# Performance work log

Measured on AMD Instinct MI355X. Metric: run time of the kernel, lower is better.

## Reference

```python
import jax, jax.numpy as jnp
import numpy as np

B, L, V, E, H, T = 64, 512, 30000, 256, 256, 9
H2 = H // 2


def setup_inputs() -> dict:
    key = jax.random.key(0)
    ks = jax.random.split(key, 16)
    s = 0.1
    sentence = jax.random.randint(ks[0], (B, L), 0, V)
    tags = jax.random.randint(ks[1], (B, L), 0, T)
    lengths = jax.random.randint(ks[2], (B,), L // 4, L + 1)
    padding_mask = (jnp.arange(L)[None, :] < lengths[:, None]).astype(jnp.int32)
    emb = jax.random.normal(ks[3], (V, E)) * s
    w_ih_f = jax.random.normal(ks[4], (4 * H2, E)) * s
    w_hh_f = jax.random.normal(ks[5], (4 * H2, H2)) * s
    b_f = jax.random.normal(ks[6], (4 * H2,)) * s
    w_ih_b = jax.random.normal(ks[7], (4 * H2, E)) * s
    w_hh_b = jax.random.normal(ks[8], (4 * H2, H2)) * s
    b_b = jax.random.normal(ks[9], (4 * H2,)) * s
    W_out = jax.random.normal(ks[10], (T, H)) * s
    b_out = jax.random.normal(ks[11], (T,)) * s
    start_trans = jax.random.normal(ks[12], (T,)) * s
    end_trans = jax.random.normal(ks[13], (T,)) * s
    trans = jax.random.normal(ks[14], (T, T)) * s
    return {"sentence": sentence, "tags": tags, "padding_mask": padding_mask,
            "batch_sequence_max_len": L, "emb": emb,
            "w_ih_f": w_ih_f, "w_hh_f": w_hh_f, "b_f": b_f,
            "w_ih_b": w_ih_b, "w_hh_b": w_hh_b, "b_b": b_b,
            "W_out": W_out, "b_out": b_out,
            "start_trans": start_trans, "end_trans": end_trans, "trans": trans}


def _lstm_dir(x, m, w_ih, w_hh, b):
    # x: [L,B,E] time-major, m: [L,B] bool. PyTorch gate order i,f,g,o.
    gx = jnp.einsum('lbe,ge->lbg', x, w_ih) + b  # precompute input contribution
    h2 = w_hh.shape[1]
    Bb = x.shape[1]

    def step(carry, inp):
        h, c = carry
        g, mt = inp
        g = g + h @ w_hh.T
        i, f, gg, o = jnp.split(g, 4, axis=-1)
        i = jax.nn.sigmoid(i); f = jax.nn.sigmoid(f)
        gg = jnp.tanh(gg); o = jax.nn.sigmoid(o)
        c_new = f * c + i * gg
        h_new = o * jnp.tanh(c_new)
        mt = mt[:, None]
        h_out = jnp.where(mt, h_new, h)
        c_out = jnp.where(mt, c_new, c)
        y = jnp.where(mt, h_new, 0.0)  # pad_packed pads outputs with 0
        return (h_out, c_out), y

    init = (jnp.zeros((Bb, h2), x.dtype), jnp.zeros((Bb, h2), x.dtype))
    _, outs = jax.lax.scan(step, init, (gx, m))
    return outs  # [L,B,H2]


def reference(sentence, tags, padding_mask, batch_sequence_max_len,
              emb, w_ih_f, w_hh_f, b_f, w_ih_b, w_hh_b, b_b,
              W_out, b_out, start_trans, end_trans, trans):
    Lm = batch_sequence_max_len
    sentence = sentence[:, :Lm]
    tags = tags[:, :Lm]
    pm = padding_mask[:, :Lm]
    Bsz = sentence.shape[0]
    bidx = jnp.arange(Bsz)

    x = jnp.swapaxes(emb[sentence], 0, 1)            # [L,B,E]
    m = jnp.swapaxes(pm, 0, 1).astype(bool)          # [L,B]
    fwd = _lstm_dir(x, m, w_ih_f, w_hh_f, b_f)
    bwd = _lstm_dir(x[::-1], m[::-1], w_ih_b, w_hh_b, b_b)[::-1]
    lstm_out = jnp.concatenate([fwd, bwd], axis=-1)  # [L,B,H]
    emissions = lstm_out @ W_out.T + b_out           # [L,B,T]

    tags_t = jnp.swapaxes(tags, 0, 1)                # [L,B]
    mf = m.astype(emissions.dtype)

    # ---- CRF numerator (gold path score) ----
    e_tag = jnp.take_along_axis(emissions, tags_t[:, :, None], axis=2)[:, :, 0]  # [L,B]
    num = start_trans[tags_t[0]] + e_tag[0]
    tr = trans[tags_t[:-1], tags_t[1:]]              # [L-1,B]
    num = num + jnp.sum((tr + e_tag[1:]) * mf[1:], axis=0)
    last_idx = jnp.sum(pm, axis=1).astype(jnp.int32) - 1
    num = num + end_trans[tags_t[last_idx, bidx]]

    # ---- CRF log-partition (forward algorithm) ----
    score0 = start_trans[None, :] + emissions[0]     # [B,T]

    def norm_step(score, inp):
        e_t, mt = inp
        nxt = jax.scipy.special.logsumexp(
            score[:, :, None] + trans[None, :, :] + e_t[:, None, :], axis=1)
        return jnp.where(mt[:, None], nxt, score), None

    score, _ = jax.lax.scan(norm_step, score0, (emissions[1:], m[1:]))
    logZ = jax.scipy.special.logsumexp(score + end_trans[None, :], axis=1)
    loss = -jnp.sum(num - logZ) / Bsz

    # ---- Viterbi decode (no mask, like module's self.crf.decode(lstm_feats)) ----
    def vit_step(score_v, e_t):
        cand = score_v[:, :, None] + trans[None, :, :] + e_t[:, None, :]  # [B,T,T]
        return jnp.max(cand, axis=1), jnp.argmax(cand, axis=1)

    vscore, hist = jax.lax.scan(vit_step, score0, emissions[1:])  # hist: [L-1,B,T]
    best_last = jnp.argmax(vscore + end_trans[None, :], axis=1)   # [B]

    def back_step(tag, h):
        return h[bidx, tag], tag

    first_tag, rest = jax.lax.scan(back_step, best_last, hist, reverse=True)
    path = jnp.concatenate([first_tag[None, :], rest], axis=0)    # [L,B]
    predict = jnp.swapaxes(path, 0, 1).astype(jnp.int32) * pm     # mask padded positions
    return loss, predict
```

## Files before the change

kernel.cpp:

```cpp
#include <hip/hip_runtime.h>
#include <math.h>

#define LSEQ 512
#define BATCH 64
#define EDIM 256
#define HD 128
#define G4 512
#define NTAG 9
#define MTOT (LSEQ*BATCH)

typedef _Float16 f16x8 __attribute__((ext_vector_type(8)));
typedef float    f32x4 __attribute__((ext_vector_type(4)));

__device__ __forceinline__ float fsig(float x){
    return __builtin_amdgcn_rcpf(1.0f + __expf(-x));
}
__device__ __forceinline__ float ftanh(float x){
    return 1.0f - 2.0f*__builtin_amdgcn_rcpf(1.0f + __expf(2.0f*x));
}
__device__ __forceinline__ void wg_barrier_lds(){
    asm volatile("s_waitcnt lgkmcnt(0)" ::: "memory");
    __builtin_amdgcn_s_barrier();
    asm volatile("" ::: "memory");
}

#define GBM 128
#define GBN 128
#define GBK 32
__global__ __launch_bounds__(256) void gx_gemm(
    const int* __restrict__ sent, const float* __restrict__ emb,
    const float* __restrict__ wf, const float* __restrict__ wb,
    const float* __restrict__ bf, const float* __restrict__ bb,
    float* __restrict__ gx)
{
    __shared__ f16x8 Ah[512], Am[512], Bh[512], Bm[512];
    __shared__ int sidx[GBM];
    const int tid = threadIdx.x;
    const int bm0 = blockIdx.x * GBM;
    const int bn0 = blockIdx.y * GBN;
    if (tid < GBM){
        int m = bm0 + tid;
        sidx[tid] = sent[(m & 63)*LSEQ + (m >> 6)];
    }
    __syncthreads();

    const float* srcA[2];
    const float* srcB[2];
    #pragma unroll
    for (int p=0;p<2;p++){
        const int d   = tid + 256*p;
        const int row = (d>>6)*16 + (d&15);
        const int kq  = (d>>4)&3;
        srcA[p] = emb + (size_t)sidx[row]*EDIM + kq*8;
        const int col = bn0 + row;
        srcB[p] = ((col < G4) ? (wf + (size_t)col*EDIM)
                              : (wb + (size_t)(col-G4)*EDIM)) + kq*8;
    }

    const int lane = tid & 63;
    const int wid  = tid >> 6;
    const int wm   = wid >> 1;
    const int wn   = wid & 1;

    f32x4 acc[4][4];
    #pragma unroll
    for (int i=0;i<4;i++)
        #pragma unroll
        for (int jj=0;jj<4;jj++)
            #pragma unroll
            for (int e=0;e<4;e++) acc[i][jj][e]=0.f;

    float4 ra[2][2], rb[2][2];
    #define LOADC(K0)  { _Pragma("unroll") for (int p=0;p<2;p++){ \
        ra[p][0] = *(const float4*)(srcA[p] + (K0));  ra[p][1] = *(const float4*)(srcA[p] + (K0) + 4); \
        rb[p][0] = *(const float4*)(srcB[p] + (K0));  rb[p][1] = *(const float4*)(srcB[p] + (K0) + 4); } }

    LOADC(0);
    for (int c=0;c<8;c++){
        wg_barrier_lds();
        #pragma unroll
        for (int p=0;p<2;p++){
            float va[8] = {ra[p][0].x, ra[p][0].y, ra[p][0].z, ra[p][0].w,
                           ra[p][1].x, ra[p][1].y, ra[p][1].z, ra[p][1].w};
            float vb[8] = {rb[p][0].x, rb[p][0].y, rb[p][0].z, rb[p][0].w,
                           rb[p][1].x, rb[p][1].y, rb[p][1].z, rb[p][1].w};
            f16x8 ahh, amm, bhh, bmm;
            #pragma unroll
            for (int i=0;i<8;i++){
                _Float16 hv = (_Float16)va[i];
                ahh[i] = hv; amm[i] = (_Float16)(va[i] - (float)hv);
                _Float16 hw = (_Float16)vb[i];
                bhh[i] = hw; bmm[i] = (_Float16)(vb[i] - (float)hw);
            }
            Ah[tid + 256*p] = ahh;  Am[tid + 256*p] = amm;
            Bh[tid + 256*p] = bhh;  Bm[tid + 256*p] = bmm;
        }
        if (c < 7) LOADC(32*(c+1));
        wg_barrier_lds();

        f16x8 ah[4], am[4];
        #pragma unroll
        for (int mt=0;mt<4;mt++){
            ah[mt] = Ah[(wm*4+mt)*64 + lane];
            am[mt] = Am[(wm*4+mt)*64 + lane];
        }
        #pragma unroll
        for (int nt=0;nt<4;nt++){
            f16x8 bh = Bh[(wn*4+nt)*64 + lane];
            f16x8 bm = Bm[(wn*4+nt)*64 + lane];
            #pragma unroll
            for (int mt=0;mt<4;mt++){
                acc[mt][nt] = __builtin_amdgcn_mfma_f32_16x16x32_f16(ah[mt], bh, acc[mt][nt], 0,0,0);
                acc[mt][nt] = __builtin_amdgcn_mfma_f32_16x16x32_f16(am[mt], bh, acc[mt][nt], 0,0,0);
                acc[mt][nt] = __builtin_amdgcn_mfma_f32_16x16x32_f16(ah[mt], bm, acc[mt][nt], 0,0,0);
            }
        }
    }
    #undef LOADC

    #pragma unroll
    for (int mt=0;mt<4;mt++){
        #pragma unroll
        for (int nt=0;nt<4;nt++){
            const int n   = bn0 + wn*64 + nt*16 + (lane & 15);
            const int dir = n >> 9;
            const int j   = n & 511;
            const float bias = (n < G4) ? bf[n] : bb[n - G4];
            const int mrow = bm0 + wm*64 + mt*16 + ((lane >> 4) << 2);
            float* o = gx + (size_t)dir*((size_t)MTOT*G4) + (size_t)mrow*G4 + j;
            o[0*G4] = acc[mt][nt][0] + bias;
            o[1*G4] = acc[mt][nt][1] + bias;
            o[2*G4] = acc[mt][nt][2] + bias;
            o[3*G4] = acc[mt][nt][3] + bias;
        }
    }
}

__global__ __launch_bounds__(512, 2) void lstm_rec(
    const float* __restrict__ gx,
    const float* __restrict__ whf, const float* __restrict__ whb,
    const int* __restrict__ pm,
    float* __restrict__ lout)
{
    const int wg  = blockIdx.x;
    const int dir = wg >> 6;
    const int b   = wg & 63;
    const int t   = threadIdx.x;
    const int kh  = t >> 8;
    const int gr  = t & 255;
    const int j   = t & 127;

    const float* wbase = dir ? whb : whf;
    float w0[64], w1[64];
    {
        const float* r0 = wbase + (size_t)gr*HD       + kh*64;
        const float* r1 = wbase + (size_t)(gr+256)*HD + kh*64;
        #pragma unroll
        for (int k=0;k<64;k+=4){
            float4 v = *(const float4*)(r0+k);
            w0[k]=v.x; w0[k+1]=v.y; w0[k+2]=v.z; w0[k+3]=v.w;
            float4 u = *(const float4*)(r1+k);
            w1[k]=u.x; w1[k+1]=u.y; w1[k+2]=u.z; w1[k+3]=u.w;
        }
    }
    __shared__ float hsh[HD];
    __shared__ float pact[2][512];
    __shared__ int   pms[LSEQ];
    for (int q=t; q<LSEQ; q+=512) pms[q] = pm[b*LSEQ + q];
    if (t < HD) hsh[t] = 0.f;
    float c = 0.f, h = 0.f;

    const size_t stepel = (size_t)BATCH*G4;
    const float* gxb = gx + (size_t)dir*((size_t)MTOT*G4) + (size_t)b*G4
                          + (dir ? (size_t)(LSEQ-1)*stepel : 0);
    const ptrdiff_t dstep = dir ? -(ptrdiff_t)stepel : (ptrdiff_t)stepel;
    float* op = lout + (size_t)b*256 + dir*HD + j;

    float4 gc = {0,0,0,0}, gn1 = {0,0,0,0};
    if (t < 128){
        gc.x  = gxb[j];          gc.y  = gxb[j+128];
        gc.z  = gxb[j+256];      gc.w  = gxb[j+384];
        const float* p1 = gxb + dstep;
        gn1.x = p1[j];           gn1.y = p1[j+128];
        gn1.z = p1[j+256];       gn1.w = p1[j+384];
    }
    wg_barrier_lds();

    for (int s=0; s<LSEQ; s++){
        float4 gn2 = {0,0,0,0};
        if (t < 128 && s+2 < LSEQ){
            const float* p = gxb + (ptrdiff_t)(s+2)*dstep;
            gn2.x = p[j]; gn2.y = p[j+128]; gn2.z = p[j+256]; gn2.w = p[j+384];
        }
        const int l = dir ? (LSEQ-1-s) : s;
        const int pmv = pms[l];

        float a0=0.f,a1=0.f,b0=0.f,b1=0.f;
        const float* hp = &hsh[kh*64];
        #pragma unroll
        for (int k=0;k<64;k+=8){
            float4 x0 = *(const float4*)(hp+k);
            float4 x1 = *(const float4*)(hp+k+4);
            a0 += x0.x*w0[k+0] + x0.y*w0[k+1] + x0.z*w0[k+2] + x0.w*w0[k+3];
            a1 += x1.x*w0[k+4] + x1.y*w0[k+5] + x1.z*w0[k+6] + x1.w*w0[k+7];
            b0 += x0.x*w1[k+0] + x0.y*w1[k+1] + x0.z*w1[k+2] + x0.w*w1[k+3];
            b1 += x1.x*w1[k+4] + x1.y*w1[k+5] + x1.z*w1[k+6] + x1.w*w1[k+7];
        }
        pact[kh][gr]     = a0 + a1;
        pact[kh][gr+256] = b0 + b1;
        wg_barrier_lds();

        if (t < 128){
            float p0 = gc.x + pact[0][j]     + pact[1][j];
            float p1 = gc.y + pact[0][j+128] + pact[1][j+128];
            float p2 = gc.z + pact[0][j+256] + pact[1][j+256];
            float p3 = gc.w + pact[0][j+384] + pact[1][j+384];
            float i_ = fsig(p0), f_ = fsig(p1), g_ = ftanh(p2), o_ = fsig(p3);
            float cn = f_*c + i_*g_;
            float hn = o_*ftanh(cn);
            float y;
            if (pmv) { c = cn; h = hn; y = hn; } else { y = 0.f; }
            hsh[j] = h;
            op[(size_t)l*(BATCH*256)] = y;
        }
        wg_barrier_lds();
        gc = gn1; gn1 = gn2;
    }
}

__global__ __launch_bounds__(256) void emis_kernel(
    const float* __restrict__ xin, const float* __restrict__ Wo,
    const float* __restrict__ bo, float* __restrict__ e)
{
    __shared__ float Wl[NTAG*260];
    const int tid = threadIdx.x;
    for (int i=tid; i<NTAG*256; i+=256) Wl[(i>>8)*260 + (i&255)] = Wo[i];
    __syncthreads();
    const int m0 = blockIdx.x * 32;
    const int tg = tid & 7;
    const int r  = tid >> 3;
    const float* xr = xin + (size_t)(m0 + r) * 256;
    float a0=0.f, a1=0.f;
    #pragma unroll 8
    for (int k=0;k<256;k+=4){
        float4 xv = *(const float4*)(xr + k);
        float4 w0 = *(const float4*)&Wl[tg*260 + k];
        a0 += xv.x*w0.x + xv.y*w0.y + xv.z*w0.z + xv.w*w0.w;
        if (tg == 0) {
            float4 w8 = *(const float4*)&Wl[8*260 + k];
            a1 += xv.x*w8.x + xv.y*w8.y + xv.z*w8.z + xv.w*w8.w;
        }
    }
    e[(size_t)(m0+r)*NTAG + tg] = a0 + bo[tg];
    if (tg == 0) e[(size_t)(m0+r)*NTAG + 8] = a1 + bo[8];
}

__global__ __launch_bounds__(64) void crf_scan(
    const float* __restrict__ e, const int* __restrict__ pm,
    const int* __restrict__ tags,
    const float* __restrict__ stt, const float* __restrict__ ent,
    const float* __restrict__ trans,
    float* __restrict__ logZ, float* __restrict__ num,
    unsigned char* __restrict__ hist, int* __restrict__ bestl)
{
    const int blk  = blockIdx.x;
    const int lane = threadIdx.x;

    if (blk < 10) {
        const int bw = lane / 9;
        const int tp = lane % 9;
        const int b  = blk * 7 + bw;
        const bool act = (bw < 7) && (b < BATCH);
        const int gbase = bw * 9;

        float trc[NTAG];
        #pragma unroll
        for (int t=0;t<NTAG;t++) trc[t] = trans[t*NTAG+tp];
        const float ent_tp = ent[tp];

        int part = 0;
        if (act) for (int l=tp; l<LSEQ; l+=NTAG) part += pm[b*LSEQ + l];
        int len = 0;
        #pragma unroll
        for (int t=0;t<NTAG;t++) len += __shfl(part, gbase + t, 64);

        float ev0 = act ? e[(size_t)b*NTAG + tp] : 0.f;
        float sn = stt[tp] + ev0;
        float sv = sn;

        float evb[8];
        #pragma unroll
        for (int q=0;q<8;q++)
            evb[q] = act ? e[((size_t)(1+q)*BATCH + b)*NTAG + tp] : 0.f;

        unsigned char* hb = hist + (size_t)b*16 + tp;

        for (int l0=1; l0<LSEQ; l0+=8){
            #pragma unroll
            for (int q=0;q<8;q++){
                const int l = l0 + q;
                if (l < LSEQ) {
                    float ev = evb[q];
                    const int lp = l + 8;
                    evb[q] = (act && lp < LSEQ) ? e[((size_t)lp*BATCH + b)*NTAG + tp] : 0.f;

                    float an[NTAG], av[NTAG];
                    #pragma unroll
                    for (int t=0;t<NTAG;t++){
                        an[t] = __shfl(sn, gbase + t, 64) + trc[t];
                        av[t] = __shfl(sv, gbase + t, 64) + trc[t];
                    }
                    float mx = an[0];
                    #pragma unroll
                    for (int t=1;t<NTAG;t++) mx = fmaxf(mx, an[t]);
                    float ss = 0.f;
                    #pragma unroll
                    for (int t=0;t<NTAG;t++) ss += __expf(an[t]-mx);
                    float nxt = mx + __logf(ss) + ev;
                    sn = (l < len) ? nxt : sn;
                    float bv = av[0]; int bi = 0;
                    #pragma unroll
                    for (int t=1;t<NTAG;t++){ if (av[t] > bv){ bv = av[t]; bi = t; } }
                    if (act) hb[(size_t)(l-1)*1024] = (unsigned char)bi;
                    sv = bv + ev;
                }
            }
        }

        float fz = sn + ent_tp;
        float fv = sv + ent_tp;
        float gz[NTAG], gv[NTAG];
        #pragma unroll
        for (int t=0;t<NTAG;t++){
            gz[t] = __shfl(fz, gbase + t, 64);
            gv[t] = __shfl(fv, gbase + t, 64);
        }
        if (act && tp == 0) {
            float mx = gz[0];
            #pragma unroll
            for (int t=1;t<NTAG;t++) mx = fmaxf(mx, gz[t]);
            float ss = 0.f;
            #pragma unroll
            for (int t=0;t<NTAG;t++) ss += __expf(gz[t]-mx);
            logZ[b] = mx + __logf(ss);
            float bv = gv[0]; int bi = 0;
            #pragma unroll
            for (int t=1;t<NTAG;t++){ if (gv[t] > bv){ bv = gv[t]; bi = t; } }
            bestl[b] = bi;
        }
    } else {
        __shared__ float trl[NTAG*NTAG];
        __shared__ float stl[NTAG], enl[NTAG];
        for (int i=lane; i<NTAG*NTAG; i+=64) trl[i] = trans[i];
        if (lane < NTAG) { stl[lane] = stt[lane]; enl[lane] = ent[lane]; }
        __syncthreads();
        const int b = lane;
        int len = 0;
        for (int l=0; l<LSEQ; l+=4){
            int4 p = *(const int4*)&pm[b*LSEQ + l];
            len += p.x + p.y + p.z + p.w;
        }
        int tprev = tags[b*LSEQ];
        float acc = stl[tprev] + e[(size_t)b*NTAG + tprev];
        #pragma unroll 4
        for (int l=1; l<len; l++){
            int tl = tags[b*LSEQ + l];
            acc += trl[tprev*NTAG + tl] + e[((size_t)l*BATCH + b)*NTAG + tl];
            tprev = tl;
        }
        acc += enl[tprev];
        num[b] = acc;
    }
}

__global__ __launch_bounds__(64) void backtrace_kernel(
    const unsigned char* __restrict__ hist, const int* __restrict__ bestl,
    const int* __restrict__ pm, const float* __restrict__ num,
    const float* __restrict__ logZ, float* __restrict__ out)
{
    const int b = threadIdx.x;
    float d = num[b] - logZ[b];
    #pragma unroll
    for (int off=32; off; off>>=1) d += __shfl_down(d, off);
    if (b == 0) out[0] = -d * (1.0f/64.0f);
    int tag = bestl[b];
    out[1 + b*LSEQ + (LSEQ-1)] = (float)(tag * pm[b*LSEQ + (LSEQ-1)]);
    #pragma unroll 8
    for (int l = LSEQ-2; l >= 0; l--) {
        uint4 row = *(const uint4*)(hist + (size_t)l*1024 + b*16);
        unsigned int wlo  = (tag & 4) ? row.y : row.x;
        unsigned int wsel = (tag & 8) ? row.z : wlo;
        tag = (int)((wsel >> ((tag & 3) * 8)) & 255u);
        out[1 + b*LSEQ + l] = (float)(tag * pm[b*LSEQ + l]);
    }
}

extern "C" void kernel_launch(void* const* d_in, const int* in_sizes, int n_in,
                              void* d_out, int out_size, void* d_ws, size_t ws_size,
                              hipStream_t stream)
{
    (void)in_sizes; (void)n_in; (void)out_size; (void)ws_size;
    const int*   sent  = (const int*)  d_in[0];
    const int*   tags  = (const int*)  d_in[1];
    const int*   pm    = (const int*)  d_in[2];
    const float* emb   = (const float*)d_in[4];
    const float* wihf  = (const float*)d_in[5];
    const float* whhf  = (const float*)d_in[6];
    const float* bf    = (const float*)d_in[7];
    const float* wihb  = (const float*)d_in[8];
    const float* whhb  = (const float*)d_in[9];
    const float* bb    = (const float*)d_in[10];
    const float* Wo    = (const float*)d_in[11];
    const float* bo    = (const float*)d_in[12];
    const float* stt   = (const float*)d_in[13];
    const float* ent   = (const float*)d_in[14];
    const float* trans = (const float*)d_in[15];

    char* ws = (char*)d_ws;
    float* gx            = (float*)(ws);
    float* lout          = (float*)(ws + 134217728);
    float* emis          = (float*)(ws + 167772160);
    unsigned char* hist  = (unsigned char*)(ws + 168951808);
    float* numb          = (float*)(ws + 169475072);
    float* logZ          = (float*)(ws + 169475328);
    int*   bestl         = (int*)  (ws + 169475584);

    dim3 g1(MTOT/GBM, (2*G4)/GBN);
    gx_gemm<<<g1, 256, 0, stream>>>(sent, emb, wihf, wihb, bf, bb, gx);
    lstm_rec<<<128, 512, 0, stream>>>(gx, whhf, whhb, pm, lout);
    emis_kernel<<<MTOT/32, 256, 0, stream>>>(lout, Wo, bo, emis);
    crf_scan<<<11, 64, 0, stream>>>(emis, pm, tags, stt, ent, trans, logZ, numb, hist, bestl);
    backtrace_kernel<<<1, 64, 0, stream>>>(hist, bestl, pm, numb, logZ, (float*)d_out);
}
```

Measured before the change: 799.0 us.

## Move LSTM recurrent weights from registers to LDS and a pre-packed global buffer

The recurrent kernel no longer keeps 128 weight floats per thread in registers. Half of the W_hh slice (k<64) is staged into a 128KB XOR-swizzled LDS array. The other half (k>=64) is read each step from a coalesced global buffer that a new pack_whh kernel fills, and which should stay resident in L2. The occupancy bound of 2 blocks per CU is dropped. The aim is to cut register pressure and likely spills, at the cost of extra LDS and L2 traffic on every step of the serial recurrence.

```diff
diff --git a/kernel.cpp b/kernel.cpp
--- a/kernel.cpp
+++ b/kernel.cpp
@@ -26,7 +26,6 @@
 
 #define GBM 128
 #define GBN 128
-#define GBK 32
 __global__ __launch_bounds__(256) void gx_gemm(
     const int* __restrict__ sent, const float* __restrict__ emb,
     const float* __restrict__ wf, const float* __restrict__ wb,
@@ -136,10 +135,24 @@
     }
 }
 
-__global__ __launch_bounds__(512, 2) void lstm_rec(
+__global__ __launch_bounds__(256) void pack_whh(
+    const float* __restrict__ whf, const float* __restrict__ whb, float4* __restrict__ sbuf)
+{
+    const int dir = blockIdx.x;
+    const int c   = blockIdx.y;
+    const int tt  = threadIdx.x;
+    const float* W = dir ? whb : whf;
+    const int row = (c < 16) ? tt : (tt + 256);
+    const int k0  = 64 + 4*(c & 15);
+    sbuf[((size_t)dir*32 + c)*256 + tt] = *(const float4*)&W[(size_t)row*HD + k0];
+}
+
+#define DOT4(W,H) ((W).x*(H).x + (W).y*(H).y + (W).z*(H).z + (W).w*(H).w)
+__global__ __launch_bounds__(512) void lstm_rec(
     const float* __restrict__ gx,
     const float* __restrict__ whf, const float* __restrict__ whb,
     const int* __restrict__ pm,
+    const float4* __restrict__ sbuf,
     float* __restrict__ lout)
 {
     const int wg  = blockIdx.x;
@@ -150,22 +163,20 @@
     const int gr  = t & 255;
     const int j   = t & 127;
 
-    const float* wbase = dir ? whb : whf;
-    float w0[64], w1[64];
-    {
-        const float* r0 = wbase + (size_t)gr*HD       + kh*64;
-        const float* r1 = wbase + (size_t)(gr+256)*HD + kh*64;
-        #pragma unroll
-        for (int k=0;k<64;k+=4){
-            float4 v = *(const float4*)(r0+k);
-            w0[k]=v.x; w0[k+1]=v.y; w0[k+2]=v.z; w0[k+3]=v.w;
-            float4 u = *(const float4*)(r1+k);
-            w1[k]=u.x; w1[k+1]=u.y; w1[k+2]=u.z; w1[k+3]=u.w;
-        }
-    }
-    __shared__ float hsh[HD];
-    __shared__ float pact[2][512];
-    __shared__ int   pms[LSEQ];
+    __shared__ float4 wl4[256*32];
+    __shared__ float  pact2[2][512];
+    __shared__ float  hsh[HD];
+    __shared__ int    pms[LSEQ];
+
+    if (t < 256){
+        const float* W = dir ? whb : whf;
+        const int sw = t & 7;
+        #pragma unroll
+        for (int i=0;i<32;i++){
+            const int row = (i < 16) ? t : (t + 256);
+            wl4[t*32 + (i ^ sw)] = *(const float4*)&W[(size_t)row*HD + 4*(i & 15)];
+        }
+    }
     for (int q=t; q<LSEQ; q+=512) pms[q] = pm[b*LSEQ + q];
     if (t < HD) hsh[t] = 0.f;
     float c = 0.f, h = 0.f;
@@ -186,6 +197,10 @@
     }
     wg_barrier_lds();
 
+    const float4* wb4 = &wl4[gr*32];
+    const int sw = gr & 7;
+    const float4* sb  = sbuf + (size_t)dir*8192 + gr;
+
     for (int s=0; s<LSEQ; s++){
         float4 gn2 = {0,0,0,0};
         if (t < 128 && s+2 < LSEQ){
@@ -195,26 +210,45 @@
         const int l = dir ? (LSEQ-1-s) : s;
         const int pmv = pms[l];
 
-        float a0=0.f,a1=0.f,b0=0.f,b1=0.f;
-        const float* hp = &hsh[kh*64];
-        #pragma unroll
-        for (int k=0;k<64;k+=8){
-            float4 x0 = *(const float4*)(hp+k);
-            float4 x1 = *(const float4*)(hp+k+4);
-            a0 += x0.x*w0[k+0] + x0.y*w0[k+1] + x0.z*w0[k+2] + x0.w*w0[k+3];
-            a1 += x1.x*w0[k+4] + x1.y*w0[k+5] + x1.z*w0[k+6] + x1.w*w0[k+7];
-            b0 += x0.x*w1[k+0] + x0.y*w1[k+1] + x0.z*w1[k+2] + x0.w*w1[k+3];
-            b1 += x1.x*w1[k+4] + x1.y*w1[k+5] + x1.z*w1[k+6] + x1.w*w1[k+7];
-        }
-        pact[kh][gr]     = a0 + a1;
-        pact[kh][gr+256] = b0 + b1;
+        float a = 0.f, bb = 0.f;
+        if (kh == 0){
+            #pragma unroll
+            for (int g=0; g<4; g++){
+                float4 h0 = *(const float4*)&hsh[g*16 +  0];
+                float4 h1 = *(const float4*)&hsh[g*16 +  4];
+                float4 h2 = *(const float4*)&hsh[g*16 +  8];
+                float4 h3 = *(const float4*)&hsh[g*16 + 12];
+                float4 wA0 = wb4[(g*4+0) ^ sw], wA1 = wb4[(g*4+1) ^ sw],
+                       wA2 = wb4[(g*4+2) ^ sw], wA3 = wb4[(g*4+3) ^ sw];
+                float4 wB0 = wb4[16 + ((g*4+0) ^ sw)], wB1 = wb4[16 + ((g*4+1) ^ sw)],
+                       wB2 = wb4[16 + ((g*4+2) ^ sw)], wB3 = wb4[16 + ((g*4+3) ^ sw)];
+                a  += (DOT4(wA0,h0)+DOT4(wA1,h1)) + (DOT4(wA2,h2)+DOT4(wA3,h3));
+                bb += (DOT4(wB0,h0)+DOT4(wB1,h1)) + (DOT4(wB2,h2)+DOT4(wB3,h3));
+            }
+        } else {
+            #pragma unroll
+            for (int g=0; g<4; g++){
+                float4 h0 = *(const float4*)&hsh[64 + g*16 +  0];
+                float4 h1 = *(const float4*)&hsh[64 + g*16 +  4];
+                float4 h2 = *(const float4*)&hsh[64 + g*16 +  8];
+                float4 h3 = *(const float4*)&hsh[64 + g*16 + 12];
+                float4 wA0 = sb[(g*4+0)*256], wA1 = sb[(g*4+1)*256],
+                       wA2 = sb[(g*4+2)*256], wA3 = sb[(g*4+3)*256];
+                float4 wB0 = sb[(16+g*4+0)*256], wB1 = sb[(16+g*4+1)*256],
+                       wB2 = sb[(16+g*4+2)*256], wB3 = sb[(16+g*4+3)*256];
+                a  += (DOT4(wA0,h0)+DOT4(wA1,h1)) + (DOT4(wA2,h2)+DOT4(wA3,h3));
+                bb += (DOT4(wB0,h0)+DOT4(wB1,h1)) + (DOT4(wB2,h2)+DOT4(wB3,h3));
+            }
+        }
+        pact2[kh][gr]     = a;
+        pact2[kh][gr+256] = bb;
         wg_barrier_lds();
 
         if (t < 128){
-            float p0 = gc.x + pact[0][j]     + pact[1][j];
-            float p1 = gc.y + pact[0][j+128] + pact[1][j+128];
-            float p2 = gc.z + pact[0][j+256] + pact[1][j+256];
-            float p3 = gc.w + pact[0][j+384] + pact[1][j+384];
+            float p0 = gc.x + pact2[0][j]     + pact2[1][j];
+            float p1 = gc.y + pact2[0][j+128] + pact2[1][j+128];
+            float p2 = gc.z + pact2[0][j+256] + pact2[1][j+256];
+            float p3 = gc.w + pact2[0][j+384] + pact2[1][j+384];
             float i_ = fsig(p0), f_ = fsig(p1), g_ = ftanh(p2), o_ = fsig(p3);
             float cn = f_*c + i_*g_;
             float hn = o_*ftanh(cn);
@@ -424,10 +458,12 @@
     float* numb          = (float*)(ws + 169475072);
     float* logZ          = (float*)(ws + 169475328);
     int*   bestl         = (int*)  (ws + 169475584);
-
+    float4* sbuf         = (float4*)(ws + 168951808);
+
+    pack_whh<<<dim3(2,32), 256, 0, stream>>>(whhf, whhb, sbuf);
     dim3 g1(MTOT/GBM, (2*G4)/GBN);
     gx_gemm<<<g1, 256, 0, stream>>>(sent, emb, wihf, wihb, bf, bb, gx);
-    lstm_rec<<<128, 512, 0, stream>>>(gx, whhf, whhb, pm, lout);
+    lstm_rec<<<128, 512, 0, stream>>>(gx, whhf, whhb, pm, sbuf, lout);
     emis_kernel<<<MTOT/32, 256, 0, stream>>>(lout, Wo, bo, emis);
     crf_scan<<<11, 64, 0, stream>>>(emis, pm, tags, stt, ent, trans, logZ, numb, hist, bestl);
     backtrace_kernel<<<1, 64, 0, stream>>>(hist, bestl, pm, numb, logZ, (float*)d_out);
```

Measured after the change: 1.326 ms. +65.9%, slower.

## Move recurrent LSTM weights from registers into LDS plus a prepacked L2 stream

Applied to the files above, without the earlier changes.

The recurrent kernel no longer holds 128 W_hh floats per thread in registers under a (512,2) launch bound, which likely forced heavy spilling. Half of each direction's W_hh now sits in a padded LDS array, and the other half is prepacked by a new pack_whh kernel into a coalesced float4 buffer that every step reads from global/L2. The reduction is split into four k-quarters with a four-way partial sum. This trades register pressure for per-step LDS and L2 traffic on the serial critical path, and it reuses the hist workspace region, which is only written after the recurrence finishes.

```diff
diff --git a/kernel.cpp b/kernel.cpp
--- a/kernel.cpp
+++ b/kernel.cpp
@@ -26,7 +26,6 @@
 
 #define GBM 128
 #define GBN 128
-#define GBK 32
 __global__ __launch_bounds__(256) void gx_gemm(
     const int* __restrict__ sent, const float* __restrict__ emb,
     const float* __restrict__ wf, const float* __restrict__ wb,
@@ -136,36 +135,49 @@
     }
 }
 
-__global__ __launch_bounds__(512, 2) void lstm_rec(
+__global__ __launch_bounds__(512) void pack_whh(
+    const float* __restrict__ whf, const float* __restrict__ whb, float4* __restrict__ sbuf)
+{
+    const int dir = blockIdx.x;
+    const int i   = blockIdx.y;
+    const int t   = threadIdx.x;
+    const float* W = dir ? whb : whf;
+    const int gr  = t & 127, kq = t >> 7;
+    const int row = gr + 128*(i >> 2);
+    const int k   = kq*32 + 16 + 4*(i & 3);
+    sbuf[((size_t)dir*16 + i)*512 + t] = *(const float4*)&W[(size_t)row*HD + k];
+}
+
+#define DOT4(W,H) ((W).x*(H).x + (W).y*(H).y + (W).z*(H).z + (W).w*(H).w)
+__global__ __launch_bounds__(512) void lstm_rec(
     const float* __restrict__ gx,
     const float* __restrict__ whf, const float* __restrict__ whb,
     const int* __restrict__ pm,
+    const float4* __restrict__ sbuf,
     float* __restrict__ lout)
 {
     const int wg  = blockIdx.x;
     const int dir = wg >> 6;
     const int b   = wg & 63;
     const int t   = threadIdx.x;
-    const int kh  = t >> 8;
-    const int gr  = t & 255;
+    const int kq  = t >> 7;
+    const int gr  = t & 127;
     const int j   = t & 127;
 
-    const float* wbase = dir ? whb : whf;
-    float w0[64], w1[64];
+    __shared__ float4 wld4[512*17];
+    __shared__ float  pact4[4][512];
+    __shared__ float  hsh[HD];
+    __shared__ int    pms[LSEQ];
+
     {
-        const float* r0 = wbase + (size_t)gr*HD       + kh*64;
-        const float* r1 = wbase + (size_t)(gr+256)*HD + kh*64;
-        #pragma unroll
-        for (int k=0;k<64;k+=4){
-            float4 v = *(const float4*)(r0+k);
-            w0[k]=v.x; w0[k+1]=v.y; w0[k+2]=v.z; w0[k+3]=v.w;
-            float4 u = *(const float4*)(r1+k);
-            w1[k]=u.x; w1[k+1]=u.y; w1[k+2]=u.z; w1[k+3]=u.w;
-        }
-    }
-    __shared__ float hsh[HD];
-    __shared__ float pact[2][512];
-    __shared__ int   pms[LSEQ];
+        const float* W = dir ? whb : whf;
+        const float* wr = &W[(size_t)t*HD];
+        #pragma unroll
+        for (int c=0;c<16;c++){
+            const int k = (c>>2)*32 + 4*(c&3);
+            wld4[t*17 + c] = *(const float4*)&wr[k];
+        }
+    }
     for (int q=t; q<LSEQ; q+=512) pms[q] = pm[b*LSEQ + q];
     if (t < HD) hsh[t] = 0.f;
     float c = 0.f, h = 0.f;
@@ -186,6 +198,8 @@
     }
     wg_barrier_lds();
 
+    const float4* sb = sbuf + (size_t)dir*16*512 + t;
+
     for (int s=0; s<LSEQ; s++){
         float4 gn2 = {0,0,0,0};
         if (t < 128 && s+2 < LSEQ){
@@ -195,26 +209,34 @@
         const int l = dir ? (LSEQ-1-s) : s;
         const int pmv = pms[l];
 
-        float a0=0.f,a1=0.f,b0=0.f,b1=0.f;
-        const float* hp = &hsh[kh*64];
-        #pragma unroll
-        for (int k=0;k<64;k+=8){
-            float4 x0 = *(const float4*)(hp+k);
-            float4 x1 = *(const float4*)(hp+k+4);
-            a0 += x0.x*w0[k+0] + x0.y*w0[k+1] + x0.z*w0[k+2] + x0.w*w0[k+3];
-            a1 += x1.x*w0[k+4] + x1.y*w0[k+5] + x1.z*w0[k+6] + x1.w*w0[k+7];
-            b0 += x0.x*w1[k+0] + x0.y*w1[k+1] + x0.z*w1[k+2] + x0.w*w1[k+3];
-            b1 += x1.x*w1[k+4] + x1.y*w1[k+5] + x1.z*w1[k+6] + x1.w*w1[k+7];
-        }
-        pact[kh][gr]     = a0 + a1;
-        pact[kh][gr+256] = b0 + b1;
+        float a0=0.f, a1=0.f, a2=0.f, a3=0.f;
+        #pragma unroll
+        for (int m=0;m<4;m++){
+            float4 hv = *(const float4*)&hsh[kq*32 + 4*m];
+            a0 += DOT4(wld4[(gr     )*17 + kq*4 + m], hv);
+            a1 += DOT4(wld4[(gr+128 )*17 + kq*4 + m], hv);
+            a2 += DOT4(wld4[(gr+256 )*17 + kq*4 + m], hv);
+            a3 += DOT4(wld4[(gr+384 )*17 + kq*4 + m], hv);
+        }
+        #pragma unroll
+        for (int m=0;m<4;m++){
+            float4 hv = *(const float4*)&hsh[kq*32 + 16 + 4*m];
+            a0 += DOT4(sb[(m    )*512], hv);
+            a1 += DOT4(sb[(4+m  )*512], hv);
+            a2 += DOT4(sb[(8+m  )*512], hv);
+            a3 += DOT4(sb[(12+m )*512], hv);
+        }
+        pact4[kq][gr]     = a0;
+        pact4[kq][gr+128] = a1;
+        pact4[kq][gr+256] = a2;
+        pact4[kq][gr+384] = a3;
         wg_barrier_lds();
 
         if (t < 128){
-            float p0 = gc.x + pact[0][j]     + pact[1][j];
-            float p1 = gc.y + pact[0][j+128] + pact[1][j+128];
-            float p2 = gc.z + pact[0][j+256] + pact[1][j+256];
-            float p3 = gc.w + pact[0][j+384] + pact[1][j+384];
+            float p0 = gc.x + ((pact4[0][j]    +pact4[1][j]    )+(pact4[2][j]    +pact4[3][j]    ));
+            float p1 = gc.y + ((pact4[0][j+128]+pact4[1][j+128])+(pact4[2][j+128]+pact4[3][j+128]));
+            float p2 = gc.z + ((pact4[0][j+256]+pact4[1][j+256])+(pact4[2][j+256]+pact4[3][j+256]));
+            float p3 = gc.w + ((pact4[0][j+384]+pact4[1][j+384])+(pact4[2][j+384]+pact4[3][j+384]));
             float i_ = fsig(p0), f_ = fsig(p1), g_ = ftanh(p2), o_ = fsig(p3);
             float cn = f_*c + i_*g_;
             float hn = o_*ftanh(cn);
@@ -424,10 +446,12 @@
     float* numb          = (float*)(ws + 169475072);
     float* logZ          = (float*)(ws + 169475328);
     int*   bestl         = (int*)  (ws + 169475584);
-
+    float4* sbuf         = (float4*)(ws + 168951808);
+
+    pack_whh<<<dim3(2,16), 512, 0, stream>>>(whhf, whhb, sbuf);
     dim3 g1(MTOT/GBM, (2*G4)/GBN);
     gx_gemm<<<g1, 256, 0, stream>>>(sent, emb, wihf, wihb, bf, bb, gx);
-    lstm_rec<<<128, 512, 0, stream>>>(gx, whhf, whhb, pm, lout);
+    lstm_rec<<<128, 512, 0, stream>>>(gx, whhf, whhb, pm, sbuf, lout);
     emis_kernel<<<MTOT/32, 256, 0, stream>>>(lout, Wo, bo, emis);
     crf_scan<<<11, 64, 0, stream>>>(emis, pm, tags, stt, ent, trans, logZ, numb, hist, bestl);
     backtrace_kernel<<<1, 64, 0, stream>>>(hist, bestl, pm, numb, logZ, (float*)d_out);
```

Result: slower. 894.4 us (+11.9%).
